# Performance work log

Hardware: AMD Instinct MI355X
Metric: run time of the kernel (lower is better)

## Reference

```python
import jax, jax.numpy as jnp
import numpy as np

# dims
B, H, W = 2, 128, 256
MD = 34            # model_dim (last 2 channels = sin/cos lat)
LD = MD - 2        # learnable_dim = 32
NH, HD = 4, 8      # n_heads, head_dim
SH = 64            # shared_hidden (DISCO out channels)
K = 25             # number of DISCO basis functions (5x5 kernel_shape)
P = 7              # local stencil width (lat x lon support of geodesic basis)
R = P // 2
FF1, FF2 = 512, 256


def setup_inputs() -> dict:
    key = jax.random.key(0)
    ks = jax.random.split(key, 16)
    x = jax.random.normal(ks[0], (B, H, W, MD), dtype=jnp.float32)
    # latitude-dependent sparse geodesic basis values over a 7x7 stencil
    psi_val = jax.random.uniform(ks[1], (K, H, P * P), dtype=jnp.float32) * 0.1
    disco_w = jax.random.normal(ks[2], (SH, K), dtype=jnp.float32) * 0.1
    disco_b = jax.random.normal(ks[3], (SH,), dtype=jnp.float32) * 0.01
    # per-head MLP: shared_hidden -> 32 -> 1
    hw1 = jax.random.normal(ks[4], (NH, SH, 32), dtype=jnp.float32) * (1.0 / np.sqrt(SH))
    hb1 = jax.random.normal(ks[5], (NH, 32), dtype=jnp.float32) * 0.01
    hw2 = jax.random.normal(ks[6], (NH, 32, 1), dtype=jnp.float32) * (1.0 / np.sqrt(32))
    hb2 = jax.random.normal(ks[7], (NH, 1), dtype=jnp.float32) * 0.01
    # FFN: model_dim -> 512 -> 256 -> learnable_dim
    fw1 = jax.random.normal(ks[8], (MD, FF1), dtype=jnp.float32) * (1.0 / np.sqrt(MD))
    fw1 = fw1.at[-2:, :].set(0.0)  # matches ffn[0].weight[:, -2:] = 0 init
    fb1 = jax.random.normal(ks[9], (FF1,), dtype=jnp.float32) * 0.01
    fw2 = jax.random.normal(ks[10], (FF1, FF2), dtype=jnp.float32) * (1.0 / np.sqrt(FF1))
    fb2 = jax.random.normal(ks[11], (FF2,), dtype=jnp.float32) * 0.01
    fw3 = jax.random.normal(ks[12], (FF2, LD), dtype=jnp.float32) * (1.0 / np.sqrt(FF2))
    fb3 = jax.random.normal(ks[13], (LD,), dtype=jnp.float32) * 0.01
    return {"x": x, "psi_val": psi_val, "disco_w": disco_w, "disco_b": disco_b,
            "hw1": hw1, "hb1": hb1, "hw2": hw2, "hb2": hb2,
            "fw1": fw1, "fb1": fb1, "fw2": fw2, "fb2": fb2, "fw3": fw3, "fb3": fb3}


def _gelu(t):
    return jax.nn.gelu(t, approximate=False)  # torch nn.GELU default (erf)


def _disco_s2(xn, psi_val, disco_w, disco_b):
    """DISCO sparse-basis conv on single-channel maps.
    xn: (N, H, W). Basis values vary with output latitude, longitude is
    translation-invariant; support is a lat-clamped / lon-wrapped 7x7 stencil.
    Returns (N, SH, H, W)."""
    xp = jnp.pad(xn, ((0, 0), (R, R), (0, 0)), mode="edge")  # clamp at poles
    shifts = []
    for dlat in range(P):
        row = xp[:, dlat:dlat + H, :]
        for dlon in range(-R, R + 1):
            shifts.append(jnp.roll(row, -dlon, axis=2))  # wrap in longitude
    xs = jnp.stack(shifts, axis=1)  # (N, P*P, H, W)
    basis = jnp.einsum("khp,nphw->nkhw", psi_val, xs)       # basis aggregation
    return jnp.einsum("fk,nkhw->nfhw", disco_w, basis) + disco_b[None, :, None, None]


def reference(x, psi_val, disco_w, disco_b, hw1, hb1, hw2, hb2,
              fw1, fb1, fw2, fb2, fw3, fb3):
    x_learn = x[..., :LD]
    sin_cos = x[..., LD:]
    x_res = x_learn
    # (B,H,W,LD) -> (B*LD, H, W): each learnable channel is a 1-channel map
    xn = x_learn.transpose(0, 3, 1, 2).reshape(B * LD, H, W)
    d = _disco_s2(xn, psi_val, disco_w, disco_b)              # (B*LD, SH, H, W)
    d = d.reshape(B, LD, SH, H, W).transpose(0, 3, 4, 1, 2)    # (B,H,W,LD,SH)
    # per-head MLP over its head_dim slice (head index is outer in LD)
    d = d.reshape(B, H, W, NH, HD, SH)
    h = _gelu(jnp.einsum("bxynds,nso->bxyndo", d, hw1) + hb1[None, None, None, :, None, :])
    h = jnp.einsum("bxyndo,noe->bxynde", h, hw2) + hb2[None, None, None, :, None, :]
    x_learn = h[..., 0].reshape(B, H, W, LD)
    x_learn = x_learn + x_res                                  # use_residual
    x_full = jnp.concatenate([x_learn, sin_cos], axis=-1)
    x_res2 = x_learn
    t = _gelu(x_full @ fw1 + fb1)
    t = _gelu(t @ fw2 + fb2)
    t = t @ fw3 + fb3                                          # dropout p=0 -> id
    x_learn = t + x_res2
    return jnp.concatenate([x_learn, sin_cos], axis=-1)
```

## Files before the change

### kernel.cpp

```cpp
#include <hip/hip_runtime.h>
#include <math.h>


typedef __attribute__((ext_vector_type(8))) short bfrag;
typedef __attribute__((ext_vector_type(4))) float ffrag;
typedef __attribute__((ext_vector_type(4))) short short4v;

union bfi4 { int4 i; bfrag b; };

__device__ __forceinline__ float gelu_f(float v) {
  const float z = v * (2.3022077484f + 0.1029451564f * v * v);
  const float e = __builtin_amdgcn_exp2f(-z);
  return v * __builtin_amdgcn_rcpf(1.0f + e);
}

__device__ __forceinline__ short f2bf(float f) {
  union { float f; unsigned u; } v; v.f = f;
  unsigned r = (v.u + 0x7fffu + ((v.u >> 16) & 1u)) >> 16;
  return (short)r;
}

__device__ __forceinline__ short f2bf_fast(float f) {
  union { float f; unsigned u; } v; v.f = f;
  return (short)((v.u + 0x8000u) >> 16);
}

__device__ __forceinline__ float bf2f(short s) {
  union { float f; unsigned u; } v;
  v.u = ((unsigned)(unsigned short)s) << 16;
  return v.f;
}

template <int CTRL>
__device__ __forceinline__ float dpp_add(float v) {
  union { float f; int i; } s, t;
  s.f = v;
  t.i = __builtin_amdgcn_update_dpp(0, s.i, CTRL, 0xf, 0xf, true);
  return v + t.f;
}
__device__ __forceinline__ float reduce16(float v) {
  v = dpp_add<0xB1>(v);
  v = dpp_add<0x4E>(v);
  v = dpp_add<0x141>(v);
  v = dpp_add<0x140>(v);
  return v;
}

__device__ __forceinline__ void st4bf(short* p, float4 v) {
  short4v s;
  s[0] = f2bf(v.x); s[1] = f2bf(v.y); s[2] = f2bf(v.z); s[3] = f2bf(v.w);
  *(short4v*)p = s;
}

__device__ __forceinline__ void tile_map(int& w0, int& b, int& h, int& lin) {
  lin  = blockIdx.x + (blockIdx.y << 3) + (blockIdx.z << 10);
  const int xcd  = lin & 7;
  const int slot = lin >> 3;
  w0 = (slot & 7) * 32;
  b  = (slot >> 3) & 1;
  h  = (xcd << 4) | (slot >> 4);
}

__global__ __launch_bounds__(256) void k01_prep(
    const float* __restrict__ psi, const float* __restrict__ dw,
    const float* __restrict__ db,
    const float* __restrict__ fw1, const float* __restrict__ fw2,
    const float* __restrict__ fw3, const float* __restrict__ hw1,
    const float* __restrict__ hb1,
    short* __restrict__ wcb, short* __restrict__ fw1s,
    short* __restrict__ fw2s, short* __restrict__ fw3s,
    float* __restrict__ hb1e) {
  __shared__ __align__(16) char sm[24832];
  const int bid = blockIdx.x;
  const int tid = threadIdx.x;

  if (bid < 512) {
    float* tileL = (float*)sm;
    float* hw1n  = (float*)(sm + 13312);
    short* tile2 = (short*)(sm + 21504);
    const int h = bid >> 2;
    const int n = bid & 3;
    const int lane = tid & 63;
    const int w = __builtin_amdgcn_readfirstlane(tid >> 6);

    for (int e = tid; e < 512; e += 256)
      ((float4*)hw1n)[e] = ((const float4*)(hw1 + n * 2048))[e];

    float dwreg[25];
#pragma unroll
    for (int kk = 0; kk < 25; ++kk) dwreg[kk] = dw[lane * 25 + kk];
    const int p0 = w * 13;
    const int pend = (p0 + 13 < 49) ? (p0 + 13) : 49;
#pragma unroll 1
    for (int p = p0; p < pend; ++p) {
      float acc = 0.f;
#pragma unroll
      for (int kk = 0; kk < 25; ++kk)
        acc += dwreg[kk] * psi[kk * 6272 + h * 49 + p];
      tileL[lane * 52 + p] = acc;
    }
    __syncthreads();

    const int o = tid & 31;
#pragma unroll 1
    for (int pp = tid >> 5; pp < 25; pp += 8) {
      const int p2 = pp * 2;
      float a0 = 0.f, a1 = 0.f;
#pragma unroll 4
      for (int f = 0; f < 64; ++f) {
        const float wv = hw1n[f * 32 + o];
        a0 += wv * tileL[f * 52 + p2];
        a1 += wv * tileL[f * 52 + p2 + 1];
      }
      tile2[o * 52 + p2] = f2bf(a0);
      if (p2 + 1 < 49) tile2[o * 52 + p2 + 1] = f2bf(a1);
    }
    __syncthreads();

    short* outp = wcb + h * 16384 + n * 4096;
    for (int idx = tid; idx < 4096; idx += 256) {
      const int jj = idx & 7, ln = (idx >> 3) & 63;
      const int nt = (idx >> 9) & 1, kt = (idx >> 10) & 1;
      const int par = idx >> 11;
      const int k = kt * 32 + ((ln >> 4) << 3) + jj;
      const int oo = nt * 16 + (ln & 15);
      const int r = k >> 3, dlt = k & 7;
      const int j = par ? (dlt - 1) : dlt;
      short v = 0;
      if (r < 7 && j >= 0 && j < 7) v = tile2[oo * 52 + r * 7 + j];
      outp[idx] = v;
    }
    return;
  }

  if (bid < 528) {
    short* S = (short*)sm;
    const int kt = bid - 512;
    const float* src = fw2 + kt * 8192;
    for (int q = tid; q < 2048; q += 256) {
      const int lin = q * 4;
      const int kk = lin >> 8, nn = lin & 255;
      st4bf(S + kk * 260 + nn, *(const float4*)(src + lin));
    }
    __syncthreads();
    short* dst = fw2s + kt * 8192;
    for (int q = tid; q < 8192; q += 256) {
      const int jj = q & 7, lane = (q >> 3) & 63, nt = q >> 9;
      const int kk = (lane >> 4) * 8 + jj, nn = nt * 16 + (lane & 15);
      dst[q] = S[kk * 260 + nn];
    }
    return;
  }

  if (bid < 530) {
    const int X = bid - 528;
    short* S = (short*)sm;
    for (int q = tid; q < 2048; q += 256) {
      const int lin = q * 4;
      const int kk = lin >> 8, nn = lin & 255;
      st4bf(S + kk * 260 + nn, *(const float4*)(fw1 + kk * 512 + X * 256 + nn));
    }
    __syncthreads();
    for (int q = tid; q < 8192; q += 256) {
      const int jj = q & 7, lane = (q >> 3) & 63, ntl = q >> 9;
      const int kk = (lane >> 4) * 8 + jj, nn = ntl * 16 + (lane & 15);
      fw1s[X * 8192 + q] = S[kk * 260 + nn];
    }
    return;
  }

  if (bid == 530) {
    short* S = (short*)sm;
    for (int q = tid; q < 2048; q += 256) {
      const int lin = q * 4;
      const int kk = lin >> 5, nn = lin & 31;
      st4bf(S + kk * 36 + nn, *(const float4*)(fw3 + lin));
    }
    __syncthreads();
    for (int q = tid; q < 8192; q += 256) {
      const int jj = q & 7, lane = (q >> 3) & 63;
      const int nt = (q >> 9) & 1, kt = q >> 10;
      const int kk = kt * 32 + (lane >> 4) * 8 + jj, nn = nt * 16 + (lane & 15);
      fw3s[q] = S[kk * 36 + nn];
    }
    return;
  }

  if (tid < 128) {
    const int n = tid >> 5, o = tid & 31;
    float acc = hb1[n * 32 + o];
#pragma unroll
    for (int s = 0; s < 64; ++s)
      acc += hw1[n * 2048 + s * 32 + o] * db[s];
    hb1e[tid] = acc;
  }
}

__global__ __launch_bounds__(256, 8) void k23_fused(
    const float* __restrict__ x,    const short* __restrict__ wcb,
    const float* __restrict__ hb1e, const float* __restrict__ hw2,
    const float* __restrict__ hb2,
    const short* __restrict__ fw1s, const short* __restrict__ fw2s,
    const short* __restrict__ fw3s,
    const float* __restrict__ fb1,  const float* __restrict__ fb2,
    const float* __restrict__ fb3,  float* __restrict__ outb) {
  __shared__ __align__(16) char smem[20384];
  short* sX = (short*)smem;
  short* sM = (short*)(smem + 18080);

  const int tid = threadIdx.x;
  int w0, b, h, lin;
  tile_map(w0, b, h, lin);

  const int lane = tid & 63, lm = lane & 15, lq = lane >> 4;
  const int n = tid >> 6;

  float hb1v[2], hw2v[2];
#pragma unroll
  for (int nt = 0; nt < 2; ++nt) {
    hb1v[nt] = hb1e[n * 32 + nt * 16 + lm];
    hw2v[nt] = hw2[n * 32 + nt * 16 + lm];
  }
  const float hb2n = hb2[n];

  {
    int4* p = (int4*)smem;
    int4 z; z.x = z.y = z.z = z.w = 0;
    for (int e = tid; e < 20384 / 16; e += 256) p[e] = z;
  }
  __syncthreads();

#pragma unroll 1
  for (int r = 0; r < 7; ++r) {
    int hr = h - 3 + r; hr = hr < 0 ? 0 : (hr > 127 ? 127 : hr);
    const float* __restrict__ xrow = x + (size_t)((b * 128 + hr) * 256) * 34;
    short* __restrict__ sxr = sX + r * 40;
    for (int e = tid; e < 39 * 16; e += 256) {
      const int c2 = e & 15;
      const int wp = e >> 4;
      const int wr = (w0 - 3 + wp) & 255;
      const float2 v = *(const float2*)&xrow[wr * 34 + c2 * 2];
      short* dp = sxr + (c2 * 2) * 280 + wp;
      dp[0]   = f2bf_fast(v.x);
      dp[280] = f2bf_fast(v.y);
    }
  }
  __syncthreads();

  const int* tpB = (const int*)sX;

#pragma unroll 1
  for (int par = 0; par < 2; ++par) {
    bfrag cw[2][2];
#pragma unroll
    for (int kt = 0; kt < 2; ++kt)
#pragma unroll
      for (int nt = 0; nt < 2; ++nt)
        cw[kt][nt] = *(const bfrag*)(wcb + h * 16384 + n * 4096 +
                         ((par * 2 + kt) * 2 + nt) * 512 + lane * 8);

#pragma unroll 1
    for (int i = 0; i < 8; ++i) {
      const int c = n * 8 + i;

      const int base0 = c * 140 + lq * 20 + lm;
      bfi4 u0, u1;
      u0.i.x = tpB[base0];      u0.i.y = tpB[base0 + 1];
      u0.i.z = tpB[base0 + 2];  u0.i.w = tpB[base0 + 3];
      u1.i.x = tpB[base0 + 80]; u1.i.y = tpB[base0 + 81];
      u1.i.z = tpB[base0 + 82]; u1.i.w = tpB[base0 + 83];

      ffrag h0 = {0.f, 0.f, 0.f, 0.f}, h1 = {0.f, 0.f, 0.f, 0.f};
      h0 = __builtin_amdgcn_mfma_f32_16x16x32_bf16(u0.b, cw[0][0], h0, 0, 0, 0);
      h0 = __builtin_amdgcn_mfma_f32_16x16x32_bf16(u1.b, cw[1][0], h0, 0, 0, 0);
      h1 = __builtin_amdgcn_mfma_f32_16x16x32_bf16(u0.b, cw[0][1], h1, 0, 0, 0);
      h1 = __builtin_amdgcn_mfma_f32_16x16x32_bf16(u1.b, cw[1][1], h1, 0, 0, 0);

#pragma unroll
      for (int rr = 0; rr < 4; ++rr) {
        float v = gelu_f(h0[rr] + hb1v[0]) * hw2v[0] +
                  gelu_f(h1[rr] + hb1v[1]) * hw2v[1];
        v = reduce16(v);
        const int p = 2 * (lq * 4 + rr) + par;
        const float res = bf2f(sX[c * 280 + 123 + p]);
        if (lm == 0) sM[p * 36 + c] = f2bf_fast(v + hb2n + res);
      }
    }
  }
  __syncthreads();

  short* sT1h = (short*)smem;
  short* sT2  = (short*)smem;
  float* sO   = (float*)smem;
  const int wave = n;
  const int koff = lq * 8;
  const int mt3 = wave & 1;
  const int nt3 = wave >> 1;
  const int col3 = nt3 * 16 + lm;
  const int pixg = (b * 128 + h) * 256 + w0;
  const int n0 = wave * 4;

  ffrag acc[2][4];
#pragma unroll
  for (int mt = 0; mt < 2; ++mt)
#pragma unroll
    for (int ni = 0; ni < 4; ++ni) acc[mt][ni] = ffrag{0.f, 0.f, 0.f, 0.f};
  const short* w2base = fw2s + n0 * 512 + lane * 8;

#pragma unroll 1
  for (int H = 0; H < 2; ++H) {
#pragma unroll
    for (int ni = 0; ni < 4; ++ni) {
      const bfrag b1f = *(const bfrag*)(fw1s +
                          (H * 16 + wave * 4 + ni) * 512 + lane * 8);
      const int ntl = wave * 4 + ni;
#pragma unroll
      for (int mt = 0; mt < 2; ++mt) {
        const bfrag aFm = *(const bfrag*)(sM + (mt * 16 + lm) * 36 + koff);
        ffrag cc = {0.f, 0.f, 0.f, 0.f};
        cc = __builtin_amdgcn_mfma_f32_16x16x32_bf16(aFm, b1f, cc, 0, 0, 0);
        const float bias = fb1[H * 256 + ntl * 16 + lm];
#pragma unroll
        for (int r = 0; r < 4; ++r) {
          const int row = mt * 16 + lq * 4 + r;
          sT1h[row * 264 + ntl * 16 + lm] = f2bf_fast(gelu_f(cc[r] + bias));
        }
      }
    }
    __syncthreads();

#pragma unroll 1
    for (int kt = 0; kt < 8; ++kt) {
      const bfrag a0 = *(const bfrag*)(sT1h + lm * 264 + kt * 32 + koff);
      const bfrag a1 = *(const bfrag*)(sT1h + (16 + lm) * 264 + kt * 32 + koff);
#pragma unroll
      for (int np = 0; np < 2; ++np) {
        const bfrag bv0 = *(const bfrag*)(w2base + (H * 8 + kt) * 8192 + (2 * np) * 512);
        const bfrag bv1 = *(const bfrag*)(w2base + (H * 8 + kt) * 8192 + (2 * np + 1) * 512);
        acc[0][2 * np]     = __builtin_amdgcn_mfma_f32_16x16x32_bf16(a0, bv0, acc[0][2 * np], 0, 0, 0);
        acc[1][2 * np]     = __builtin_amdgcn_mfma_f32_16x16x32_bf16(a1, bv0, acc[1][2 * np], 0, 0, 0);
        acc[0][2 * np + 1] = __builtin_amdgcn_mfma_f32_16x16x32_bf16(a0, bv1, acc[0][2 * np + 1], 0, 0, 0);
        acc[1][2 * np + 1] = __builtin_amdgcn_mfma_f32_16x16x32_bf16(a1, bv1, acc[1][2 * np + 1], 0, 0, 0);
      }
    }
    __syncthreads();
  }

#pragma unroll
  for (int mt = 0; mt < 2; ++mt)
#pragma unroll
    for (int ni = 0; ni < 4; ++ni) {
      const int col = (n0 + ni) * 16 + lm;
      const float bias = fb2[col];
#pragma unroll
      for (int r = 0; r < 4; ++r) {
        const int row = mt * 16 + lq * 4 + r;
        sT2[row * 264 + col] = f2bf_fast(gelu_f(acc[mt][ni][r] + bias));
      }
    }
  __syncthreads();

  ffrag c3 = {0.f, 0.f, 0.f, 0.f};
  const short* sA3 = sT2 + (mt3 * 16 + lm) * 264 + koff;
#pragma unroll
  for (int kt = 0; kt < 8; ++kt) {
    const bfrag a = *(const bfrag*)(sA3 + kt * 32);
    const bfrag bw = *(const bfrag*)(fw3s + nt3 * 512 + kt * 1024 + lane * 8);
    c3 = __builtin_amdgcn_mfma_f32_16x16x32_bf16(a, bw, c3, 0, 0, 0);
  }
  __syncthreads();
  {
    const float bias = fb3[col3];
#pragma unroll
    for (int r = 0; r < 4; ++r) {
      const int row = mt3 * 16 + lq * 4 + r;
      const float res = bf2f(sM[row * 36 + col3]);
      sO[row * 34 + col3] = c3[r] + bias + res;
    }
  }
  if (tid < 32) {
    const float2 scv =
        *(const float2*)&x[(size_t)(((b * 128 + h) * 256 + w0 + tid)) * 34 + 32];
    sO[tid * 34 + 32] = scv.x;
    sO[tid * 34 + 33] = scv.y;
  }
  __syncthreads();
  {
    const float4* sp = (const float4*)sO;
    float4* dp = (float4*)(outb + (size_t)pixg * 34);
    for (int e = tid; e < 272; e += 256) dp[e] = sp[e];
  }
}

extern "C" void kernel_launch(void* const* d_in, const int* in_sizes, int n_in,
                              void* d_out, int out_size, void* d_ws, size_t ws_size,
                              hipStream_t stream) {
  const float* x   = (const float*)d_in[0];
  const float* psi = (const float*)d_in[1];
  const float* dw  = (const float*)d_in[2];
  const float* db  = (const float*)d_in[3];
  const float* hw1 = (const float*)d_in[4];
  const float* hb1 = (const float*)d_in[5];
  const float* hw2 = (const float*)d_in[6];
  const float* hb2 = (const float*)d_in[7];
  const float* fw1 = (const float*)d_in[8];
  const float* fb1 = (const float*)d_in[9];
  const float* fw2 = (const float*)d_in[10];
  const float* fb2 = (const float*)d_in[11];
  const float* fw3 = (const float*)d_in[12];
  const float* fb3 = (const float*)d_in[13];
  float* outb = (float*)d_out;

  short* wcb  = (short*)d_ws;
  short* fw1s = wcb + 2097152;
  short* fw2s = fw1s + 16384;
  short* fw3s = fw2s + 131072;
  float* hb1e = (float*)(fw3s + 8192);

  hipLaunchKernelGGL(k01_prep, dim3(532), dim3(256), 0, stream,
                     psi, dw, db, fw1, fw2, fw3, hw1, hb1,
                     wcb, fw1s, fw2s, fw3s, hb1e);
  hipLaunchKernelGGL(k23_fused, dim3(8, 128, 2), dim3(256), 0, stream,
                     x, wcb, hb1e, hw2, hb2,
                     fw1s, fw2s, fw3s, fb1, fb2, fb3, outb);
}
```

Before: 166.3 us.

## Swap MFMA operand order so outputs land transposed for packed stores and cheaper reductions

Swaps the A/B operands of the MFMAs in the DISCO head MLP and the FFN layers, so each lane holds four consecutive output channels of one pixel instead of four pixels of one channel. Head reductions then become in-lane sums plus two ds_bpermute steps instead of a four-step DPP reduction, and the FFN activations are written as packed bf16 int2 stores with float4 bias loads. The input row staging order is permuted to match the new B-fragment layout. The prep kernel's dot products gain split accumulators for more ILP. The main risk is subtle layout or indexing errors in the interleaved row slots and the residual offset.

```diff
diff --git a/kernel.cpp b/kernel.cpp
--- a/kernel.cpp
+++ b/kernel.cpp
@@ -31,19 +31,9 @@
   return v.f;
 }
 
-template <int CTRL>
-__device__ __forceinline__ float dpp_add(float v) {
-  union { float f; int i; } s, t;
-  s.f = v;
-  t.i = __builtin_amdgcn_update_dpp(0, s.i, CTRL, 0xf, 0xf, true);
-  return v + t.f;
-}
-__device__ __forceinline__ float reduce16(float v) {
-  v = dpp_add<0xB1>(v);
-  v = dpp_add<0x4E>(v);
-  v = dpp_add<0x141>(v);
-  v = dpp_add<0x140>(v);
-  return v;
+__device__ __forceinline__ int pkbf(float a, float b) {
+  union { float f; unsigned u; } va, vb; va.f = a; vb.f = b;
+  return (int)__builtin_amdgcn_perm(vb.u + 0x8000u, va.u + 0x8000u, 0x07060302u);
 }
 
 __device__ __forceinline__ void st4bf(short* p, float4 v) {
@@ -93,11 +83,14 @@
     const int pend = (p0 + 13 < 49) ? (p0 + 13) : 49;
 #pragma unroll 1
     for (int p = p0; p < pend; ++p) {
-      float acc = 0.f;
-#pragma unroll
-      for (int kk = 0; kk < 25; ++kk)
-        acc += dwreg[kk] * psi[kk * 6272 + h * 49 + p];
-      tileL[lane * 52 + p] = acc;
+      float ae = 0.f, ao = 0.f;
+#pragma unroll
+      for (int kk = 0; kk < 24; kk += 2) {
+        ae += dwreg[kk]     * psi[kk * 6272 + h * 49 + p];
+        ao += dwreg[kk + 1] * psi[(kk + 1) * 6272 + h * 49 + p];
+      }
+      ae += dwreg[24] * psi[24 * 6272 + h * 49 + p];
+      tileL[lane * 52 + p] = ae + ao;
     }
     __syncthreads();
 
@@ -105,15 +98,18 @@
 #pragma unroll 1
     for (int pp = tid >> 5; pp < 25; pp += 8) {
       const int p2 = pp * 2;
-      float a0 = 0.f, a1 = 0.f;
+      float a0 = 0.f, a1 = 0.f, a2 = 0.f, a3 = 0.f;
 #pragma unroll 4
-      for (int f = 0; f < 64; ++f) {
-        const float wv = hw1n[f * 32 + o];
-        a0 += wv * tileL[f * 52 + p2];
-        a1 += wv * tileL[f * 52 + p2 + 1];
+      for (int f = 0; f < 64; f += 2) {
+        const float wv0 = hw1n[f * 32 + o];
+        const float wv1 = hw1n[(f + 1) * 32 + o];
+        a0 += wv0 * tileL[f * 52 + p2];
+        a1 += wv0 * tileL[f * 52 + p2 + 1];
+        a2 += wv1 * tileL[(f + 1) * 52 + p2];
+        a3 += wv1 * tileL[(f + 1) * 52 + p2 + 1];
       }
-      tile2[o * 52 + p2] = f2bf(a0);
-      if (p2 + 1 < 49) tile2[o * 52 + p2 + 1] = f2bf(a1);
+      tile2[o * 52 + p2] = f2bf(a0 + a2);
+      if (p2 + 1 < 49) tile2[o * 52 + p2 + 1] = f2bf(a1 + a3);
     }
     __syncthreads();
 
@@ -214,13 +210,9 @@
 
   const int lane = tid & 63, lm = lane & 15, lq = lane >> 4;
   const int n = tid >> 6;
-
-  float hb1v[2], hw2v[2];
-#pragma unroll
-  for (int nt = 0; nt < 2; ++nt) {
-    hb1v[nt] = hb1e[n * 32 + nt * 16 + lm];
-    hw2v[nt] = hw2[n * 32 + nt * 16 + lm];
-  }
+  const int idx16 = (lane ^ 16) << 2;
+  const int idx32 = (lane ^ 32) << 2;
+
   const float hb2n = hb2[n];
 
   {
@@ -233,8 +225,9 @@
 #pragma unroll 1
   for (int r = 0; r < 7; ++r) {
     int hr = h - 3 + r; hr = hr < 0 ? 0 : (hr > 127 ? 127 : hr);
+    const int slot = (r < 4) ? (2 * r) : (2 * r - 7);
     const float* __restrict__ xrow = x + (size_t)((b * 128 + hr) * 256) * 34;
-    short* __restrict__ sxr = sX + r * 40;
+    short* __restrict__ sxr = sX + slot * 40;
     for (int e = tid; e < 39 * 16; e += 256) {
       const int c2 = e & 15;
       const int wp = e >> 4;
@@ -258,33 +251,46 @@
       for (int nt = 0; nt < 2; ++nt)
         cw[kt][nt] = *(const bfrag*)(wcb + h * 16384 + n * 4096 +
                          ((par * 2 + kt) * 2 + nt) * 512 + lane * 8);
+    const float4 b0v = *(const float4*)(hb1e + n * 32 + lq * 4);
+    const float4 b1v = *(const float4*)(hb1e + n * 32 + 16 + lq * 4);
+    const float4 w0v = *(const float4*)(hw2 + n * 32 + lq * 4);
+    const float4 w1v = *(const float4*)(hw2 + n * 32 + 16 + lq * 4);
 
 #pragma unroll 1
     for (int i = 0; i < 8; ++i) {
       const int c = n * 8 + i;
 
-      const int base0 = c * 140 + lq * 20 + lm;
+      const int base0 = c * 140 + lq * 40 + lm;
       bfi4 u0, u1;
       u0.i.x = tpB[base0];      u0.i.y = tpB[base0 + 1];
       u0.i.z = tpB[base0 + 2];  u0.i.w = tpB[base0 + 3];
-      u1.i.x = tpB[base0 + 80]; u1.i.y = tpB[base0 + 81];
-      u1.i.z = tpB[base0 + 82]; u1.i.w = tpB[base0 + 83];
+      u1.i.x = tpB[base0 + 20]; u1.i.y = tpB[base0 + 21];
+      u1.i.z = tpB[base0 + 22]; u1.i.w = tpB[base0 + 23];
 
       ffrag h0 = {0.f, 0.f, 0.f, 0.f}, h1 = {0.f, 0.f, 0.f, 0.f};
-      h0 = __builtin_amdgcn_mfma_f32_16x16x32_bf16(u0.b, cw[0][0], h0, 0, 0, 0);
-      h0 = __builtin_amdgcn_mfma_f32_16x16x32_bf16(u1.b, cw[1][0], h0, 0, 0, 0);
-      h1 = __builtin_amdgcn_mfma_f32_16x16x32_bf16(u0.b, cw[0][1], h1, 0, 0, 0);
-      h1 = __builtin_amdgcn_mfma_f32_16x16x32_bf16(u1.b, cw[1][1], h1, 0, 0, 0);
-
-#pragma unroll
-      for (int rr = 0; rr < 4; ++rr) {
-        float v = gelu_f(h0[rr] + hb1v[0]) * hw2v[0] +
-                  gelu_f(h1[rr] + hb1v[1]) * hw2v[1];
-        v = reduce16(v);
-        const int p = 2 * (lq * 4 + rr) + par;
-        const float res = bf2f(sX[c * 280 + 123 + p]);
-        if (lm == 0) sM[p * 36 + c] = f2bf_fast(v + hb2n + res);
-      }
+      h0 = __builtin_amdgcn_mfma_f32_16x16x32_bf16(cw[0][0], u0.b, h0, 0, 0, 0);
+      h0 = __builtin_amdgcn_mfma_f32_16x16x32_bf16(cw[1][0], u1.b, h0, 0, 0, 0);
+      h1 = __builtin_amdgcn_mfma_f32_16x16x32_bf16(cw[0][1], u0.b, h1, 0, 0, 0);
+      h1 = __builtin_amdgcn_mfma_f32_16x16x32_bf16(cw[1][1], u1.b, h1, 0, 0, 0);
+
+      float s0 = gelu_f(h0[0] + b0v.x) * w0v.x;
+      s0 += gelu_f(h0[1] + b0v.y) * w0v.y;
+      s0 += gelu_f(h0[2] + b0v.z) * w0v.z;
+      s0 += gelu_f(h0[3] + b0v.w) * w0v.w;
+      float s1 = gelu_f(h1[0] + b1v.x) * w1v.x;
+      s1 += gelu_f(h1[1] + b1v.y) * w1v.y;
+      s1 += gelu_f(h1[2] + b1v.z) * w1v.z;
+      s1 += gelu_f(h1[3] + b1v.w) * w1v.w;
+      union { float f; int i; } sv, t1, t2;
+      sv.f = s0 + s1;
+      t1.i = __builtin_amdgcn_ds_bpermute(idx16, sv.i);
+      sv.f += t1.f;
+      t2.i = __builtin_amdgcn_ds_bpermute(idx32, sv.i);
+      const float tot = sv.f + t2.f;
+
+      const int p = 2 * lm + par;
+      const float res = bf2f(sX[c * 280 + 243 + p]);
+      if (lq == 0) sM[p * 36 + c] = f2bf_fast(tot + hb2n + res);
     }
   }
   __syncthreads();
@@ -314,17 +320,16 @@
       const bfrag b1f = *(const bfrag*)(fw1s +
                           (H * 16 + wave * 4 + ni) * 512 + lane * 8);
       const int ntl = wave * 4 + ni;
+      const float4 fb1v = *(const float4*)(fb1 + H * 256 + ntl * 16 + lq * 4);
 #pragma unroll
       for (int mt = 0; mt < 2; ++mt) {
         const bfrag aFm = *(const bfrag*)(sM + (mt * 16 + lm) * 36 + koff);
         ffrag cc = {0.f, 0.f, 0.f, 0.f};
-        cc = __builtin_amdgcn_mfma_f32_16x16x32_bf16(aFm, b1f, cc, 0, 0, 0);
-        const float bias = fb1[H * 256 + ntl * 16 + lm];
-#pragma unroll
-        for (int r = 0; r < 4; ++r) {
-          const int row = mt * 16 + lq * 4 + r;
-          sT1h[row * 264 + ntl * 16 + lm] = f2bf_fast(gelu_f(cc[r] + bias));
-        }
+        cc = __builtin_amdgcn_mfma_f32_16x16x32_bf16(b1f, aFm, cc, 0, 0, 0);
+        int2 wv;
+        wv.x = pkbf(gelu_f(cc[0] + fb1v.x), gelu_f(cc[1] + fb1v.y));
+        wv.y = pkbf(gelu_f(cc[2] + fb1v.z), gelu_f(cc[3] + fb1v.w));
+        *(int2*)(sT1h + (mt * 16 + lm) * 264 + ntl * 16 + lq * 4) = wv;
       }
     }
     __syncthreads();
@@ -337,10 +342,10 @@
       for (int np = 0; np < 2; ++np) {
         const bfrag bv0 = *(const bfrag*)(w2base + (H * 8 + kt) * 8192 + (2 * np) * 512);
         const bfrag bv1 = *(const bfrag*)(w2base + (H * 8 + kt) * 8192 + (2 * np + 1) * 512);
-        acc[0][2 * np]     = __builtin_amdgcn_mfma_f32_16x16x32_bf16(a0, bv0, acc[0][2 * np], 0, 0, 0);
-        acc[1][2 * np]     = __builtin_amdgcn_mfma_f32_16x16x32_bf16(a1, bv0, acc[1][2 * np], 0, 0, 0);
-        acc[0][2 * np + 1] = __builtin_amdgcn_mfma_f32_16x16x32_bf16(a0, bv1, acc[0][2 * np + 1], 0, 0, 0);
-        acc[1][2 * np + 1] = __builtin_amdgcn_mfma_f32_16x16x32_bf16(a1, bv1, acc[1][2 * np + 1], 0, 0, 0);
+        acc[0][2 * np]     = __builtin_amdgcn_mfma_f32_16x16x32_bf16(bv0, a0, acc[0][2 * np], 0, 0, 0);
+        acc[1][2 * np]     = __builtin_amdgcn_mfma_f32_16x16x32_bf16(bv0, a1, acc[1][2 * np], 0, 0, 0);
+        acc[0][2 * np + 1] = __builtin_amdgcn_mfma_f32_16x16x32_bf16(bv1, a0, acc[0][2 * np + 1], 0, 0, 0);
+        acc[1][2 * np + 1] = __builtin_amdgcn_mfma_f32_16x16x32_bf16(bv1, a1, acc[1][2 * np + 1], 0, 0, 0);
       }
     }
     __syncthreads();
@@ -350,13 +355,11 @@
   for (int mt = 0; mt < 2; ++mt)
 #pragma unroll
     for (int ni = 0; ni < 4; ++ni) {
-      const int col = (n0 + ni) * 16 + lm;
-      const float bias = fb2[col];
-#pragma unroll
-      for (int r = 0; r < 4; ++r) {
-        const int row = mt * 16 + lq * 4 + r;
-        sT2[row * 264 + col] = f2bf_fast(gelu_f(acc[mt][ni][r] + bias));
-      }
+      const float4 fb2v = *(const float4*)(fb2 + (n0 + ni) * 16 + lq * 4);
+      int2 wv;
+      wv.x = pkbf(gelu_f(acc[mt][ni][0] + fb2v.x), gelu_f(acc[mt][ni][1] + fb2v.y));
+      wv.y = pkbf(gelu_f(acc[mt][ni][2] + fb2v.z), gelu_f(acc[mt][ni][3] + fb2v.w));
+      *(int2*)(sT2 + (mt * 16 + lm) * 264 + (n0 + ni) * 16 + lq * 4) = wv;
     }
   __syncthreads();
 
```

Result: faster. 161.1 us (-3.1%).
